# Performance work log

Measured on AMD Instinct MI355X. Metric: run time of the kernel, lower is better.

## Reference

```python
import jax, jax.numpy as jnp
import numpy as np

B = 8192; L = 50; D_EMB = 128
N_USER = 100000; N_MOVIE = 50000; N_DENSE = 8
D = 2 * D_EMB + D_EMB + N_DENSE  # 392 total_input_dim
E = 4; T = 2; H1 = 256; H2 = 128; ATT_H = 64; N_CROSS = 3


def setup_inputs() -> dict:
    key = jax.random.key(0)
    ks = jax.random.split(key, 28)
    rn = lambda k, shape, s=0.02: jax.random.normal(k, shape, jnp.float32) * s
    inp = {
        'userId': jax.random.randint(ks[0], (B,), 0, N_USER),
        'movieId': jax.random.randint(ks[1], (B,), 0, N_MOVIE),
        'seq_history': jax.random.randint(ks[2], (B, L), 0, N_MOVIE),
        'dense_feats': jax.random.normal(ks[3], (B, N_DENSE), jnp.float32),
        # embeddings (row 0 is padding_idx -> zeros)
        'emb_user': rn(ks[4], (N_USER + 1, D_EMB)).at[0].set(0.0),
        'emb_movie': rn(ks[5], (N_MOVIE + 1, D_EMB)).at[0].set(0.0),
        # DIN attention MLP: input [q,k,q-k,q*k] = 4*D_EMB
        'att_w1': rn(ks[6], (4 * D_EMB, ATT_H)), 'att_b1': jnp.zeros((ATT_H,), jnp.float32),
        'att_w2': rn(ks[7], (ATT_H, 1)), 'att_b2': jnp.zeros((1,), jnp.float32),
        # LayerNorms
        'in_gamma': jnp.ones((D,), jnp.float32), 'in_beta': jnp.zeros((D,), jnp.float32),
        'cr_gamma': jnp.ones((D,), jnp.float32), 'cr_beta': jnp.zeros((D,), jnp.float32),
        # CrossNetV2: x_{l+1} = x0 * (x_l W_l + b_l) + x_l
        'cross_W': rn(ks[8], (N_CROSS, D, D)), 'cross_b': jnp.zeros((N_CROSS, D), jnp.float32),
        # MMoE experts: Linear(D,H1)-ReLU-Linear(H1,H2), batched over E
        'exp_w1': rn(ks[9], (E, D, H1)), 'exp_b1': jnp.zeros((E, H1), jnp.float32),
        'exp_w2': rn(ks[10], (E, H1, H2)), 'exp_b2': jnp.zeros((E, H2), jnp.float32),
        # gates per task
        'gate_w': rn(ks[11], (T, D, E)), 'gate_b': jnp.zeros((T, E), jnp.float32),
        # task heads Linear(H2, 1)
        'head_w': rn(ks[12], (T, H2)), 'head_b': jnp.zeros((T,), jnp.float32),
    }
    return inp


def _layernorm(x, g, b, eps=1e-5):
    m = jnp.mean(x, axis=-1, keepdims=True)
    v = jnp.var(x, axis=-1, keepdims=True)
    return (x - m) * jax.lax.rsqrt(v + eps) * g + b


def _forward(userId, movieId, seq_history, dense_feats, emb_user, emb_movie,
             att_w1, att_b1, att_w2, att_b2, in_gamma, in_beta,
             cross_W, cross_b, cr_gamma, cr_beta,
             exp_w1, exp_b1, exp_w2, exp_b2, gate_w, gate_b, head_w, head_b):
    # sparse embedding gathers
    user_e = emb_user[userId]            # [B, D_EMB]
    movie_e = emb_movie[movieId]         # [B, D_EMB]  (target item)
    hist = emb_movie[seq_history]        # [B, L, D_EMB]
    mask = seq_history > 0               # [B, L]

    # DIN attention pooling
    q = jnp.broadcast_to(movie_e[:, None, :], hist.shape)            # [B, L, D_EMB]
    att_in = jnp.concatenate([q, hist, q - hist, q * hist], axis=-1)  # [B, L, 4*D_EMB]
    scores = (jax.nn.relu(att_in @ att_w1 + att_b1) @ att_w2 + att_b2)[..., 0]  # [B, L]
    scores = jnp.where(mask, scores, -1e9)
    probs = jax.nn.softmax(scores, axis=-1)                           # [B, L]
    interest = jnp.einsum('bl,bld->bd', probs, hist)                  # [B, D_EMB]

    x = jnp.concatenate([user_e, movie_e, interest, dense_feats], axis=-1)  # [B, D]
    x = _layernorm(x, in_gamma, in_beta)

    # CrossNetV2
    x0 = x
    for l in range(N_CROSS):
        x = x0 * (x @ cross_W[l] + cross_b[l]) + x
    x = _layernorm(x, cr_gamma, cr_beta)

    # MMoE: batched expert GEMMs + per-task soft gates
    h = jax.nn.relu(jnp.einsum('bd,edh->ebh', x, exp_w1) + exp_b1[:, None, :])  # [E,B,H1]
    eo = jnp.einsum('ebh,eho->ebo', h, exp_w2) + exp_b2[:, None, :]             # [E,B,H2]
    g = jax.nn.softmax(jnp.einsum('bd,tde->tbe', x, gate_w) + gate_b[:, None, :], axis=-1)  # [T,B,E]
    task_feat = jnp.einsum('tbe,ebo->tbo', g, eo)                                # [T,B,H2]

    logits = jnp.einsum('tbo,to->tb', task_feat, head_w) + head_b[:, None]       # [T,B]
    return logits


def reference(userId, movieId, seq_history, dense_feats, emb_user, emb_movie,
              att_w1, att_b1, att_w2, att_b2, in_gamma, in_beta,
              cross_W, cross_b, cr_gamma, cr_beta,
              exp_w1, exp_b1, exp_w2, exp_b2, gate_w, gate_b, head_w, head_b):
    return _forward(userId, movieId, seq_history, dense_feats, emb_user, emb_movie,
                    att_w1, att_b1, att_w2, att_b2, in_gamma, in_beta,
                    cross_W, cross_b, cr_gamma, cr_beta,
                    exp_w1, exp_b1, exp_w2, exp_b2, gate_w, gate_b, head_w, head_b)
```

## Files before the change

### kernel.cpp

```cpp
#include <hip/hip_runtime.h>
#include <hip/hip_bf16.h>

typedef short short8 __attribute__((ext_vector_type(8)));
typedef short short4v __attribute__((ext_vector_type(4)));
typedef float f32x4 __attribute__((ext_vector_type(4)));

constexpr int BB = 8192;
constexpr int LL = 50;
constexpr int DE = 128;
constexpr int DD = 392;
constexpr int HH1 = 256;
constexpr int HH2 = 128;

__device__ __forceinline__ short f2b(float x) {
    __hip_bfloat16 h = __float2bfloat16(x);
    return __builtin_bit_cast(short, h);
}
__device__ __forceinline__ float b2f(short v) {
    unsigned u = ((unsigned)(unsigned short)v) << 16;
    return __builtin_bit_cast(float, u);
}

__global__ __launch_bounds__(256) void prep_small(
    const float* __restrict__ w1,
    const float* __restrict__ w2, const float* __restrict__ b2,
    const float* __restrict__ head_w,
    short* __restrict__ WqpT, float* __restrict__ WkpFf,
    float* __restrict__ hw2, float* __restrict__ hc)
{
    __shared__ float hw[256];
    const int b = blockIdx.x, t = threadIdx.x;
    if (b < 32) {
        int o = b * 256 + t;
        int h = o >> 7, d = o & 127;
        WqpT[o] = f2b(w1[d * 64 + h] + w1[16384 + d * 64 + h]);
    } else if (b < 64) {
        int o = (b - 32) * 256 + t;
        int e = o & 7, lane = (o >> 3) & 63, nt = (o >> 9) & 3, kt = o >> 11;
        int k = (kt << 5) + ((lane >> 4) << 3) + e;
        int h = (nt << 4) + (lane & 15);
        int base = (o >> 3) << 4;
        WkpFf[base + e]     = w1[(128 + k) * 64 + h] - w1[(256 + k) * 64 + h];
        WkpFf[base + 8 + e] = w1[(384 + k) * 64 + h];
    } else {
        const int e = b - 64;
        hw[t] = head_w[t];
        __syncthreads();
        const float* row = &w2[((long)e * HH1 + t) * HH2];
        float s0 = 0.f, s1 = 0.f;
        #pragma unroll 8
        for (int o = 0; o < 128; o += 4) {
            float4 v = *reinterpret_cast<const float4*>(&row[o]);
            s0 += v.x * hw[o] + v.y * hw[o + 1] + v.z * hw[o + 2] + v.w * hw[o + 3];
            s1 += v.x * hw[128 + o] + v.y * hw[129 + o] + v.z * hw[130 + o] + v.w * hw[131 + o];
        }
        hw2[(((e << 8) + t) << 1) + 0] = s0;
        hw2[(((e << 8) + t) << 1) + 1] = s1;
        if (t < 2) {
            float s = 0.f;
            for (int o = 0; o < 128; ++o) s += b2[e * 128 + o] * hw[t * 128 + o];
            hc[e * 2 + t] = s;
        }
    }
}

constexpr int S0 = 3 * 392 * 392;
constexpr int S1 = 4 * 392 * 256;
constexpr int S2 = (50001 * 128) / 4;
constexpr int S3 = (BB * 128) / 4;

__global__ __launch_bounds__(256) void prep_trans(
    const float* __restrict__ cross_W, const float* __restrict__ exp_w1,
    const float* __restrict__ emb_movie, const int* __restrict__ movieId,
    short* __restrict__ WTc, short* __restrict__ WT1, short* __restrict__ embB,
    short* __restrict__ qb)
{
    int idx = blockIdx.x * 256 + threadIdx.x;
    if (idx < S0) {
        int z = idx / (392 * 392), rr = idx - z * 392 * 392;
        int c = rr / 392, r = rr - c * 392;
        WTc[idx] = f2b(cross_W[(long)z * 153664 + r * 392 + c]);
    } else if (idx < S0 + S1) {
        int j = idx - S0;
        int z = j / 100352, rr = j - z * 100352;
        int c = rr / 392, r = rr - c * 392;
        WT1[j] = f2b(exp_w1[(long)z * 100352 + r * 256 + c]);
    } else if (idx < S0 + S1 + S2) {
        long j = (long)(idx - S0 - S1) << 2;
        float4 v = *reinterpret_cast<const float4*>(&emb_movie[j]);
        short4v o;
        o[0] = f2b(v.x); o[1] = f2b(v.y); o[2] = f2b(v.z); o[3] = f2b(v.w);
        *reinterpret_cast<short4v*>(&embB[j]) = o;
    } else if (idx < S0 + S1 + S2 + S3) {
        int j = idx - S0 - S1 - S2;
        int bb = j >> 5, d0 = (j & 31) << 2;
        float4 v = *reinterpret_cast<const float4*>(
            &emb_movie[(long)movieId[bb] * DE + d0]);
        short4v o;
        o[0] = f2b(v.x); o[1] = f2b(v.y); o[2] = f2b(v.z); o[3] = f2b(v.w);
        *reinterpret_cast<short4v*>(&qb[bb * DE + d0]) = o;
    }
}

__global__ __launch_bounds__(256, 8) void attn_kernel(
    const int* __restrict__ userId, const int* __restrict__ movieId,
    const int* __restrict__ seq, const float* __restrict__ dense,
    const float* __restrict__ emb_user, const float* __restrict__ emb_movie,
    const short* __restrict__ embB,
    const float* __restrict__ qcAll, const float* __restrict__ WkpFf,
    const float* __restrict__ att_w2, const float* __restrict__ att_b2,
    const float* __restrict__ in_gamma, const float* __restrict__ in_beta,
    float* __restrict__ x0f, short* __restrict__ x0b)
{
    __shared__ short hist[64 * 128];
    __shared__ float qs[128];
    __shared__ int   seq_s[64];
    __shared__ float spS[4][64];
    __shared__ float probs[64];
    __shared__ float ibuf[4][128];
    __shared__ float stats[2];

    const int b = blockIdx.x;
    const int t = threadIdx.x;
    const int lane = t & 63;
    const int w = t >> 6;

    if (t < 128) qs[t] = emb_movie[(long)movieId[b] * DE + t];
    if (t < 64)  seq_s[t] = (t < LL) ? seq[b * LL + t] : 0;
    __syncthreads();

    #pragma unroll
    for (int i = 0; i < 4; ++i) {
        const int idx = t + (i << 8);
        const int l = idx >> 4, c = idx & 15;
        short8 hv = *reinterpret_cast<const short8*>(&embB[(long)seq_s[l] * DE + (c << 3)]);
        const int byte = (l << 8) + ((c << 4) ^ ((l & 7) << 4));
        *reinterpret_cast<short8*>(reinterpret_cast<char*>(hist) + byte) = hv;
    }

    const int col = (w << 4) + (lane & 15);
    float ue = (t < 128) ? emb_user[(long)userId[b] * DE + t] : 0.f;
    float dv = (t >= 128 && t < 136) ? dense[b * 8 + (t - 128)] : 0.f;
    const float qc  = qcAll[((long)b << 6) + col];
    const float w2v = att_w2[col];

    short8 bfrag[4];
    #pragma unroll
    for (int kt = 0; kt < 4; ++kt) {
        const float* wkp = &WkpFf[((((kt << 2) + w) << 6) | lane) << 4];
        const int kq = (kt << 5) + ((lane >> 4) << 3);
        #pragma unroll
        for (int j = 0; j < 8; ++j)
            bfrag[kt][j] = f2b(fmaf(qs[kq + j], wkp[8 + j], wkp[j]));
    }
    __syncthreads();

    #pragma unroll
    for (int mt = 0; mt < 4; ++mt) {
        f32x4 acc = {0.f, 0.f, 0.f, 0.f};
        const int row = (mt << 4) + (lane & 15);
        const int rbase = row << 8;
        const int swz = (row & 7) << 4;
        #pragma unroll
        for (int kt = 0; kt < 4; ++kt) {
            const int kbyte = (kt << 6) + ((lane >> 4) << 4);
            short8 a = *reinterpret_cast<const short8*>(
                reinterpret_cast<char*>(hist) + rbase + (kbyte ^ swz));
            acc = __builtin_amdgcn_mfma_f32_16x16x32_bf16(a, bfrag[kt], acc, 0, 0, 0);
        }
        #pragma unroll
        for (int r = 0; r < 4; ++r) {
            float v = fmaxf(acc[r] + qc, 0.f) * w2v;
            v += __shfl_xor(v, 1); v += __shfl_xor(v, 2);
            v += __shfl_xor(v, 4); v += __shfl_xor(v, 8);
            if ((lane & 15) == 0)
                spS[w][(mt << 4) + ((lane >> 4) << 2) + r] = v;
        }
    }
    __syncthreads();

    if (t < 64) {
        float sc = spS[0][t] + spS[1][t] + spS[2][t] + spS[3][t] + att_b2[0];
        float s = (t < LL) ? ((seq_s[t] > 0) ? sc : -1e9f) : -INFINITY;
        float m = s;
        #pragma unroll
        for (int off = 32; off > 0; off >>= 1) m = fmaxf(m, __shfl_xor(m, off));
        float e = (t < LL) ? __expf(s - m) : 0.f;
        float sum = e;
        #pragma unroll
        for (int off = 32; off > 0; off >>= 1) sum += __shfl_xor(sum, off);
        probs[t] = (t < LL) ? (e / sum) : 0.f;
    }
    __syncthreads();

    const int g  = t >> 5;
    const int d0 = (t & 31) << 2;
    float4 ps = make_float4(0.f, 0.f, 0.f, 0.f);
    #pragma unroll
    for (int i = 0; i < 8; ++i) {
        const int l = g + (i << 3);
        const int byte = (l << 8) + ((d0 << 1) ^ ((l & 7) << 4));
        short4v hv = *reinterpret_cast<const short4v*>(
            reinterpret_cast<const char*>(hist) + byte);
        const float p = probs[l];
        ps.x = fmaf(p, b2f(hv[0]), ps.x);
        ps.y = fmaf(p, b2f(hv[1]), ps.y);
        ps.z = fmaf(p, b2f(hv[2]), ps.z);
        ps.w = fmaf(p, b2f(hv[3]), ps.w);
    }
    ps.x += __shfl_xor(ps.x, 32); ps.y += __shfl_xor(ps.y, 32);
    ps.z += __shfl_xor(ps.z, 32); ps.w += __shfl_xor(ps.w, 32);
    if (lane < 32)
        *reinterpret_cast<float4*>(&ibuf[w][lane << 2]) = ps;
    __syncthreads();

    float v0 = (t < 128) ? ue : qs[t - 128];
    float v1 = 0.f;
    if (t < 128)       v1 = ibuf[0][t] + ibuf[1][t] + ibuf[2][t] + ibuf[3][t];
    else if (t < 136)  v1 = dv;

    float s2 = v0 + v1, q2 = v0 * v0 + v1 * v1;
    #pragma unroll
    for (int off = 32; off > 0; off >>= 1) {
        s2 += __shfl_xor(s2, off);
        q2 += __shfl_xor(q2, off);
    }
    if (lane == 0) { spS[0][w] = s2; spS[1][w] = q2; }
    __syncthreads();
    if (t == 0) {
        float S = spS[0][0] + spS[0][1] + spS[0][2] + spS[0][3];
        float Q = spS[1][0] + spS[1][1] + spS[1][2] + spS[1][3];
        float mean = S / (float)DD;
        float var = Q / (float)DD - mean * mean;
        stats[0] = mean;
        stats[1] = rsqrtf(var + 1e-5f);
    }
    __syncthreads();
    const float mean = stats[0], inv = stats[1];
    const long base = (long)b * DD;
    float o0 = (v0 - mean) * inv * in_gamma[t] + in_beta[t];
    x0f[base + t] = o0; x0b[base + t] = f2b(o0);
    if (t < 136) {
        float o1 = (v1 - mean) * inv * in_gamma[256 + t] + in_beta[256 + t];
        x0f[base + 256 + t] = o1; x0b[base + 256 + t] = f2b(o1);
    }
}

template<int MODE, int WF32, int WB16, int NXB, int NZB>
__global__ __launch_bounds__(256) void bgemm(
    const short* __restrict__ A, const short* __restrict__ WT,
    const float* __restrict__ bias,
    float* __restrict__ outF, short* __restrict__ outB,
    const float* __restrict__ x0, const float* __restrict__ xin,
    int M, int N, int K, long aZ, long wZ, long bZ, long oZ)
{
    __shared__ short As[2][64 * 64];
    __shared__ short Bs[2][64 * 64];

    int id = blockIdx.x;
    const int qq = (int)gridDim.x >> 3;
    id = (id & 7) * qq + (id >> 3);
    const int mb  = id / (NXB * NZB);
    const int rem = id - mb * (NXB * NZB);
    const int z   = rem / NXB;
    const int xb  = rem - z * NXB;

    A += (long)z * aZ; WT += (long)z * wZ; bias += (long)z * bZ;
    const long oz = (long)z * oZ;

    const int t = threadIdx.x, w = t >> 6, lane = t & 63;
    const int m0 = mb * 64, n0 = xb * 64;
    const int sm = t >> 3, sk8 = (t & 7) << 3;

    f32x4 acc[4];
    #pragma unroll
    for (int i = 0; i < 4; ++i) {
        #pragma unroll
        for (int r = 0; r < 4; ++r) acc[i][r] = 0.f;
    }

    const int nsteps = (K + 63) >> 6;
    short8 avA[2], bvA[2], avB[2], bvB[2];

    auto loadA = [&](int k0) {
        #pragma unroll
        for (int i = 0; i < 2; ++i) {
            const int r = sm + (i << 5);
            short8 zv = {0, 0, 0, 0, 0, 0, 0, 0};
            avA[i] = zv; bvA[i] = zv;
            if (k0 + sk8 < K) {
                avA[i] = *reinterpret_cast<const short8*>(&A[(long)(m0 + r) * K + k0 + sk8]);
                if (n0 + r < N)
                    bvA[i] = *reinterpret_cast<const short8*>(&WT[(long)(n0 + r) * K + k0 + sk8]);
            }
        }
    };
    auto loadB = [&](int k0) {
        #pragma unroll
        for (int i = 0; i < 2; ++i) {
            const int r = sm + (i << 5);
            short8 zv = {0, 0, 0, 0, 0, 0, 0, 0};
            avB[i] = zv; bvB[i] = zv;
            if (k0 + sk8 < K) {
                avB[i] = *reinterpret_cast<const short8*>(&A[(long)(m0 + r) * K + k0 + sk8]);
                if (n0 + r < N)
                    bvB[i] = *reinterpret_cast<const short8*>(&WT[(long)(n0 + r) * K + k0 + sk8]);
            }
        }
    };
    auto wrA = [&](int buf) {
        #pragma unroll
        for (int i = 0; i < 2; ++i) {
            const int r = sm + (i << 5);
            const int byte = (r << 7) + ((sk8 << 1) ^ ((r & 7) << 4));
            *reinterpret_cast<short8*>(reinterpret_cast<char*>(&As[buf][0]) + byte) = avA[i];
            *reinterpret_cast<short8*>(reinterpret_cast<char*>(&Bs[buf][0]) + byte) = bvA[i];
        }
    };
    auto wrB = [&](int buf) {
        #pragma unroll
        for (int i = 0; i < 2; ++i) {
            const int r = sm + (i << 5);
            const int byte = (r << 7) + ((sk8 << 1) ^ ((r & 7) << 4));
            *reinterpret_cast<short8*>(reinterpret_cast<char*>(&As[buf][0]) + byte) = avB[i];
            *reinterpret_cast<short8*>(reinterpret_cast<char*>(&Bs[buf][0]) + byte) = bvB[i];
        }
    };
    auto domfma = [&](int buf) {
        #pragma unroll
        for (int kt = 0; kt < 2; ++kt) {
            const int kbyte = (kt << 6) + ((lane >> 4) << 4);
            const int ar = (w << 4) + (lane & 15);
            short8 a = *reinterpret_cast<const short8*>(
                reinterpret_cast<char*>(&As[buf][0]) + (ar << 7) + (kbyte ^ ((ar & 7) << 4)));
            #pragma unroll
            for (int nt = 0; nt < 4; ++nt) {
                const int br = (nt << 4) + (lane & 15);
                short8 bb = *reinterpret_cast<const short8*>(
                    reinterpret_cast<char*>(&Bs[buf][0]) + (br << 7) + (kbyte ^ ((br & 7) << 4)));
                acc[nt] = __builtin_amdgcn_mfma_f32_16x16x32_bf16(a, bb, acc[nt], 0, 0, 0);
            }
        }
    };

    loadA(0);
    wrA(0);
    if (nsteps > 1) loadA(64);
    if (nsteps > 2) loadB(128);
    __syncthreads();

    int cur = 0, s = 0;
    while (s + 1 < nsteps) {
        domfma(cur);
        wrA(cur ^ 1);
        if (s + 3 < nsteps) loadA((s + 3) << 6);
        __syncthreads(); cur ^= 1; ++s;
        if (s + 1 < nsteps) {
            domfma(cur);
            wrB(cur ^ 1);
            if (s + 3 < nsteps) loadB((s + 3) << 6);
            __syncthreads(); cur ^= 1; ++s;
        }
    }
    domfma(cur);

    #pragma unroll
    for (int nt = 0; nt < 4; ++nt) {
        const int col = n0 + (nt << 4) + (lane & 15);
        if (col < N) {
            const float bv = bias[col];
            #pragma unroll
            for (int r = 0; r < 4; ++r) {
                const int row = m0 + (w << 4) + ((lane >> 4) << 2) + r;
                float v = acc[nt][r] + bv;
                if (MODE == 1) v = fmaxf(v, 0.f);
                const long o = (long)row * N + col;
                if (MODE == 2) v = x0[o] * v + xin[o];
                if (WF32) outF[oz + o] = v;
                if (WB16) outB[oz + o] = f2b(v);
            }
        }
    }
}

__global__ __launch_bounds__(256) void ln_kernel(
    const float* __restrict__ in,
    const float* __restrict__ gamma, const float* __restrict__ beta,
    float* __restrict__ outF, short* __restrict__ outB)
{
    __shared__ float red[2][4];
    __shared__ float stats[2];
    const int b = blockIdx.x, t = threadIdx.x, lane = t & 63, w = t >> 6;
    const long base = (long)b * DD;
    float v0 = in[base + t];
    float v1 = (t < 136) ? in[base + 256 + t] : 0.f;
    float s = v0 + v1, q2 = v0 * v0 + v1 * v1;
    #pragma unroll
    for (int off = 32; off > 0; off >>= 1) {
        s += __shfl_xor(s, off);
        q2 += __shfl_xor(q2, off);
    }
    if (lane == 0) { red[0][w] = s; red[1][w] = q2; }
    __syncthreads();
    if (t == 0) {
        float S = red[0][0] + red[0][1] + red[0][2] + red[0][3];
        float Q = red[1][0] + red[1][1] + red[1][2] + red[1][3];
        float mean = S / (float)DD;
        float var = Q / (float)DD - mean * mean;
        stats[0] = mean;
        stats[1] = rsqrtf(var + 1e-5f);
    }
    __syncthreads();
    const float mean = stats[0], inv = stats[1];
    float o0 = (v0 - mean) * inv * gamma[t] + beta[t];
    outF[base + t] = o0; outB[base + t] = f2b(o0);
    if (t < 136) {
        float o1 = (v1 - mean) * inv * gamma[256 + t] + beta[256 + t];
        outF[base + 256 + t] = o1; outB[base + 256 + t] = f2b(o1);
    }
}

__global__ __launch_bounds__(256) void final_kernel(
    const float* __restrict__ x, const short* __restrict__ h1,
    const float* __restrict__ hw2, const float* __restrict__ hc,
    const float* __restrict__ gate_w, const float* __restrict__ gate_b,
    const float* __restrict__ head_b, float* __restrict__ out)
{
    const int t = threadIdx.x, lane = t & 63, w = t >> 6;
    const int b = blockIdx.x * 4 + w;
    const float* xr = x + (long)b * DD;

    float xv[7];
    #pragma unroll
    for (int i = 0; i < 7; ++i) {
        int d = lane + (i << 6);
        xv[i] = (d < DD) ? xr[d] : 0.f;
    }

    float gl[8] = {0.f, 0.f, 0.f, 0.f, 0.f, 0.f, 0.f, 0.f};
    #pragma unroll
    for (int i = 0; i < 7; ++i) {
        int d = lane + (i << 6);
        if (d < DD) {
            float4 g0 = *reinterpret_cast<const float4*>(&gate_w[d << 2]);
            float4 g1 = *reinterpret_cast<const float4*>(&gate_w[1568 + (d << 2)]);
            gl[0] = fmaf(xv[i], g0.x, gl[0]); gl[1] = fmaf(xv[i], g0.y, gl[1]);
            gl[2] = fmaf(xv[i], g0.z, gl[2]); gl[3] = fmaf(xv[i], g0.w, gl[3]);
            gl[4] = fmaf(xv[i], g1.x, gl[4]); gl[5] = fmaf(xv[i], g1.y, gl[5]);
            gl[6] = fmaf(xv[i], g1.z, gl[6]); gl[7] = fmaf(xv[i], g1.w, gl[7]);
        }
    }

    float ed[8];
    #pragma unroll
    for (int e = 0; e < 4; ++e) {
        short4v hv = *reinterpret_cast<const short4v*>(
            &h1[((long)e * BB + b) * HH1 + (lane << 2)]);
        const float* hwp = &hw2[(((e << 8) + (lane << 2))) << 1];
        float4 w01 = *reinterpret_cast<const float4*>(hwp);
        float4 w23 = *reinterpret_cast<const float4*>(hwp + 4);
        float h0 = b2f(hv[0]), h1f = b2f(hv[1]), h2 = b2f(hv[2]), h3 = b2f(hv[3]);
        ed[e]     = fmaf(h0, w01.x, fmaf(h1f, w01.z, fmaf(h2, w23.x, h3 * w23.z)));
        ed[4 + e] = fmaf(h0, w01.y, fmaf(h1f, w01.w, fmaf(h2, w23.y, h3 * w23.w)));
    }

    #pragma unroll
    for (int v = 0; v < 8; ++v) {
        #pragma unroll
        for (int off = 32; off > 0; off >>= 1) {
            gl[v] += __shfl_xor(gl[v], off);
            ed[v] += __shfl_xor(ed[v], off);
        }
    }

    if (lane == 0) {
        float res[2];
        #pragma unroll
        for (int tt = 0; tt < 2; ++tt) {
            float lv[4], m = -1e30f;
            #pragma unroll
            for (int e = 0; e < 4; ++e) {
                lv[e] = gl[tt * 4 + e] + gate_b[tt * 4 + e];
                m = fmaxf(m, lv[e]);
            }
            float sum = 0.f, acc = 0.f;
            #pragma unroll
            for (int e = 0; e < 4; ++e) { lv[e] = __expf(lv[e] - m); sum += lv[e]; }
            #pragma unroll
            for (int e = 0; e < 4; ++e)
                acc = fmaf(lv[e], ed[tt * 4 + e] + hc[e * 2 + tt], acc);
            res[tt] = head_b[tt] + acc / sum;
        }
        out[b] = res[0];
        out[BB + b] = res[1];
    }
}

extern "C" void kernel_launch(void* const* d_in, const int* in_sizes, int n_in,
                              void* d_out, int out_size, void* d_ws, size_t ws_size,
                              hipStream_t stream) {
    const int*   userId    = (const int*)d_in[0];
    const int*   movieId   = (const int*)d_in[1];
    const int*   seq       = (const int*)d_in[2];
    const float* dense     = (const float*)d_in[3];
    const float* emb_user  = (const float*)d_in[4];
    const float* emb_movie = (const float*)d_in[5];
    const float* att_w1    = (const float*)d_in[6];
    const float* att_b1    = (const float*)d_in[7];
    const float* att_w2    = (const float*)d_in[8];
    const float* att_b2    = (const float*)d_in[9];
    const float* in_gamma  = (const float*)d_in[10];
    const float* in_beta   = (const float*)d_in[11];
    const float* cr_gamma  = (const float*)d_in[12];
    const float* cr_beta   = (const float*)d_in[13];
    const float* cross_W   = (const float*)d_in[14];
    const float* cross_b   = (const float*)d_in[15];
    const float* exp_w1    = (const float*)d_in[16];
    const float* exp_b1    = (const float*)d_in[17];
    const float* exp_w2    = (const float*)d_in[18];
    const float* exp_b2    = (const float*)d_in[19];
    const float* gate_w    = (const float*)d_in[20];
    const float* gate_b    = (const float*)d_in[21];
    const float* head_w    = (const float*)d_in[22];
    const float* head_b    = (const float*)d_in[23];
    float* outp = (float*)d_out;

    char* p = (char*)d_ws;
    auto alloc = [&](size_t bytes) -> char* {
        char* r = p; p += (bytes + 255) & ~(size_t)255; return r;
    };
    short* WqpT  = (short*)alloc(8192 * 2);
    float* WkpFf = (float*)alloc(16384 * 4);
    float* hw2 = (float*)alloc(2048 * 4);
    float* hc  = (float*)alloc(8 * 4);
    short* WTc = (short*)alloc((size_t)3 * 392 * 392 * 2);
    short* WT1 = (short*)alloc((size_t)4 * 256 * 392 * 2);
    short* embB = (short*)alloc((size_t)50001 * 128 * 2);
    short* qb   = (short*)alloc((size_t)BB * DE * 2);
    float* qcAll = (float*)alloc((size_t)BB * 64 * 4);
    float* x0f = (float*)alloc((size_t)BB * DD * 4);
    short* x0b = (short*)alloc((size_t)BB * DD * 2);
    float* xAf = (float*)alloc((size_t)BB * DD * 4);
    short* xAb = (short*)alloc((size_t)BB * DD * 2);
    float* xBf = (float*)alloc((size_t)BB * DD * 4);
    short* xBb = (short*)alloc((size_t)BB * DD * 2);
    short* h1b = (short*)alloc((size_t)4 * BB * HH1 * 2);

    prep_small<<<68, 256, 0, stream>>>(att_w1, exp_w2, exp_b2, head_w,
                                       WqpT, WkpFf, hw2, hc);
    prep_trans<<<(S0 + S1 + S2 + S3 + 255) / 256, 256, 0, stream>>>(
        cross_W, exp_w1, emb_movie, movieId, WTc, WT1, embB, qb);

    bgemm<0, 1, 0, 1, 1><<<128, 256, 0, stream>>>(
        qb, WqpT, att_b1, qcAll, nullptr, nullptr, nullptr,
        BB, 64, DE, 0, 0, 0, 0);

    attn_kernel<<<BB, 256, 0, stream>>>(userId, movieId, seq, dense,
                                        emb_user, emb_movie, embB,
                                        qcAll, WkpFf,
                                        att_w2, att_b2,
                                        in_gamma, in_beta, x0f, x0b);

    bgemm<2, 1, 1, 7, 1><<<896, 256, 0, stream>>>(x0b, WTc, cross_b, xAf, xAb,
                                                  x0f, x0f, BB, DD, DD, 0, 0, 0, 0);
    bgemm<2, 1, 1, 7, 1><<<896, 256, 0, stream>>>(xAb, WTc + 392 * 392, cross_b + 392,
                                                  xBf, xBb, x0f, xAf, BB, DD, DD, 0, 0, 0, 0);
    bgemm<2, 1, 0, 7, 1><<<896, 256, 0, stream>>>(xBb, WTc + 2 * 392 * 392, cross_b + 784,
                                                  xAf, nullptr, x0f, xBf, BB, DD, DD, 0, 0, 0, 0);

    ln_kernel<<<BB, 256, 0, stream>>>(xAf, cr_gamma, cr_beta, xBf, xBb);

    bgemm<1, 0, 1, 4, 4><<<2048, 256, 0, stream>>>(
        xBb, WT1, exp_b1, nullptr, h1b, nullptr, nullptr,
        BB, HH1, DD, 0, (long)HH1 * DD, HH1, (long)BB * HH1);

    final_kernel<<<BB / 4, 256, 0, stream>>>(xBf, h1b, hw2, hc,
                                             gate_w, gate_b, head_b, outp);

    (void)in_sizes; (void)n_in; (void)out_size; (void)ws_size;
}
```

Before: 177.2 us.

## Fuse last cross layer with LayerNorm and gate logits; trim attention and GEMM pipeline

Measured after the change: 182.3 us. 1.03x slower.

```diff
diff --git a/kernel.cpp b/kernel.cpp
--- a/kernel.cpp
+++ b/kernel.cpp
@@ -64,16 +64,17 @@
     }
 }
 
-constexpr int S0 = 3 * 392 * 392;
+constexpr int S0 = 2 * 392 * 392;
 constexpr int S1 = 4 * 392 * 256;
 constexpr int S2 = (50001 * 128) / 4;
 constexpr int S3 = (BB * 128) / 4;
+constexpr int S4 = 400 * 448;
 
 __global__ __launch_bounds__(256) void prep_trans(
     const float* __restrict__ cross_W, const float* __restrict__ exp_w1,
     const float* __restrict__ emb_movie, const int* __restrict__ movieId,
     short* __restrict__ WTc, short* __restrict__ WT1, short* __restrict__ embB,
-    short* __restrict__ qb)
+    short* __restrict__ qb, short* __restrict__ WT3)
 {
     int idx = blockIdx.x * 256 + threadIdx.x;
     if (idx < S0) {
@@ -99,6 +100,11 @@
         short4v o;
         o[0] = f2b(v.x); o[1] = f2b(v.y); o[2] = f2b(v.z); o[3] = f2b(v.w);
         *reinterpret_cast<short4v*>(&qb[bb * DE + d0]) = o;
+    } else if (idx < S0 + S1 + S2 + S3 + S4) {
+        int j = idx - S0 - S1 - S2 - S3;
+        int n = j / 448, k = j - n * 448;
+        WT3[j] = (n < 392 && k < 392)
+                 ? f2b(cross_W[2L * 153664 + (long)k * 392 + n]) : (short)0;
     }
 }
 
@@ -112,30 +118,36 @@
     const float* __restrict__ in_gamma, const float* __restrict__ in_beta,
     float* __restrict__ x0f, short* __restrict__ x0b)
 {
-    __shared__ short hist[64 * 128];
-    __shared__ float qs[128];
-    __shared__ int   seq_s[64];
-    __shared__ float spS[4][64];
-    __shared__ float probs[64];
-    __shared__ float ibuf[4][128];
-    __shared__ float stats[2];
+    __shared__ __align__(16) char lds[17408];
+    short* hist = reinterpret_cast<short*>(lds);
+    float* qs   = reinterpret_cast<float*>(lds + 13312);
+    float* spS  = reinterpret_cast<float*>(lds + 13824);
+    float* probs= reinterpret_cast<float*>(lds + 14848);
+    float* ibuf = reinterpret_cast<float*>(lds + 15104);
+    float* stats= reinterpret_cast<float*>(lds + 17152);
 
     const int b = blockIdx.x;
     const int t = threadIdx.x;
     const int lane = t & 63;
     const int w = t >> 6;
-
-    if (t < 128) qs[t] = emb_movie[(long)movieId[b] * DE + t];
-    if (t < 64)  seq_s[t] = (t < LL) ? seq[b * LL + t] : 0;
-    __syncthreads();
-
+    const int mid = movieId[b];
+
+    if (t < 32)
+        *reinterpret_cast<float4*>(&qs[t << 2]) =
+            *reinterpret_cast<const float4*>(&emb_movie[(long)mid * DE + (t << 2)]);
+
+    const int g0 = t >> 4, c = t & 15;
     #pragma unroll
     for (int i = 0; i < 4; ++i) {
-        const int idx = t + (i << 8);
-        const int l = idx >> 4, c = idx & 15;
-        short8 hv = *reinterpret_cast<const short8*>(&embB[(long)seq_s[l] * DE + (c << 3)]);
-        const int byte = (l << 8) + ((c << 4) ^ ((l & 7) << 4));
-        *reinterpret_cast<short8*>(reinterpret_cast<char*>(hist) + byte) = hv;
+        const int l = g0 + (i << 4);
+        if (l < 52) {
+            int sidx = (l < LL) ? (b * LL + l) : 0;
+            int sv = seq[sidx];
+            if (l >= LL) sv = 0;
+            short8 hv = *reinterpret_cast<const short8*>(&embB[(long)sv * DE + (c << 3)]);
+            const int byte = (l << 8) + ((c << 4) ^ ((l & 7) << 4));
+            *reinterpret_cast<short8*>(reinterpret_cast<char*>(hist) + byte) = hv;
+        }
     }
 
     const int col = (w << 4) + (lane & 15);
@@ -143,6 +155,10 @@
     float dv = (t >= 128 && t < 136) ? dense[b * 8 + (t - 128)] : 0.f;
     const float qc  = qcAll[((long)b << 6) + col];
     const float w2v = att_w2[col];
+    int mseq = 0;
+    if (t < LL) mseq = seq[b * LL + t];
+
+    __syncthreads();
 
     short8 bfrag[4];
     #pragma unroll
@@ -153,7 +169,6 @@
         for (int j = 0; j < 8; ++j)
             bfrag[kt][j] = f2b(fmaf(qs[kq + j], wkp[8 + j], wkp[j]));
     }
-    __syncthreads();
 
     #pragma unroll
     for (int mt = 0; mt < 4; ++mt) {
@@ -174,14 +189,14 @@
             v += __shfl_xor(v, 1); v += __shfl_xor(v, 2);
             v += __shfl_xor(v, 4); v += __shfl_xor(v, 8);
             if ((lane & 15) == 0)
-                spS[w][(mt << 4) + ((lane >> 4) << 2) + r] = v;
+                spS[(w << 6) + (mt << 4) + ((lane >> 4) << 2) + r] = v;
         }
     }
     __syncthreads();
 
     if (t < 64) {
-        float sc = spS[0][t] + spS[1][t] + spS[2][t] + spS[3][t] + att_b2[0];
-        float s = (t < LL) ? ((seq_s[t] > 0) ? sc : -1e9f) : -INFINITY;
+        float sc = spS[t] + spS[64 + t] + spS[128 + t] + spS[192 + t] + att_b2[0];
+        float s = (t < LL) ? ((mseq > 0) ? sc : -1e9f) : -INFINITY;
         float m = s;
         #pragma unroll
         for (int off = 32; off > 0; off >>= 1) m = fmaxf(m, __shfl_xor(m, off));
@@ -199,24 +214,26 @@
     #pragma unroll
     for (int i = 0; i < 8; ++i) {
         const int l = g + (i << 3);
-        const int byte = (l << 8) + ((d0 << 1) ^ ((l & 7) << 4));
-        short4v hv = *reinterpret_cast<const short4v*>(
-            reinterpret_cast<const char*>(hist) + byte);
-        const float p = probs[l];
-        ps.x = fmaf(p, b2f(hv[0]), ps.x);
-        ps.y = fmaf(p, b2f(hv[1]), ps.y);
-        ps.z = fmaf(p, b2f(hv[2]), ps.z);
-        ps.w = fmaf(p, b2f(hv[3]), ps.w);
+        if (l < LL) {
+            const int byte = (l << 8) + ((d0 << 1) ^ ((l & 7) << 4));
+            short4v hv = *reinterpret_cast<const short4v*>(
+                reinterpret_cast<const char*>(hist) + byte);
+            const float p = probs[l];
+            ps.x = fmaf(p, b2f(hv[0]), ps.x);
+            ps.y = fmaf(p, b2f(hv[1]), ps.y);
+            ps.z = fmaf(p, b2f(hv[2]), ps.z);
+            ps.w = fmaf(p, b2f(hv[3]), ps.w);
+        }
     }
     ps.x += __shfl_xor(ps.x, 32); ps.y += __shfl_xor(ps.y, 32);
     ps.z += __shfl_xor(ps.z, 32); ps.w += __shfl_xor(ps.w, 32);
     if (lane < 32)
-        *reinterpret_cast<float4*>(&ibuf[w][lane << 2]) = ps;
+        *reinterpret_cast<float4*>(&ibuf[(w << 7) + ((lane & 31) << 2)]) = ps;
     __syncthreads();
 
     float v0 = (t < 128) ? ue : qs[t - 128];
     float v1 = 0.f;
-    if (t < 128)       v1 = ibuf[0][t] + ibuf[1][t] + ibuf[2][t] + ibuf[3][t];
+    if (t < 128)       v1 = ibuf[t] + ibuf[128 + t] + ibuf[256 + t] + ibuf[384 + t];
     else if (t < 136)  v1 = dv;
 
     float s2 = v0 + v1, q2 = v0 * v0 + v1 * v1;
@@ -225,11 +242,11 @@
         s2 += __shfl_xor(s2, off);
         q2 += __shfl_xor(q2, off);
     }
-    if (lane == 0) { spS[0][w] = s2; spS[1][w] = q2; }
+    if (lane == 0) { spS[w] = s2; spS[64 + w] = q2; }
     __syncthreads();
     if (t == 0) {
-        float S = spS[0][0] + spS[0][1] + spS[0][2] + spS[0][3];
-        float Q = spS[1][0] + spS[1][1] + spS[1][2] + spS[1][3];
+        float S = spS[0] + spS[1] + spS[2] + spS[3];
+        float Q = spS[64] + spS[65] + spS[66] + spS[67];
         float mean = S / (float)DD;
         float var = Q / (float)DD - mean * mean;
         stats[0] = mean;
@@ -280,7 +297,7 @@
     }
 
     const int nsteps = (K + 63) >> 6;
-    short8 avA[2], bvA[2], avB[2], bvB[2];
+    short8 avA[2], bvA[2];
 
     auto loadA = [&](int k0) {
         #pragma unroll
@@ -295,19 +312,6 @@
             }
         }
     };
-    auto loadB = [&](int k0) {
-        #pragma unroll
-        for (int i = 0; i < 2; ++i) {
-            const int r = sm + (i << 5);
-            short8 zv = {0, 0, 0, 0, 0, 0, 0, 0};
-            avB[i] = zv; bvB[i] = zv;
-            if (k0 + sk8 < K) {
-                avB[i] = *reinterpret_cast<const short8*>(&A[(long)(m0 + r) * K + k0 + sk8]);
-                if (n0 + r < N)
-                    bvB[i] = *reinterpret_cast<const short8*>(&WT[(long)(n0 + r) * K + k0 + sk8]);
-            }
-        }
-    };
     auto wrA = [&](int buf) {
         #pragma unroll
         for (int i = 0; i < 2; ++i) {
@@ -315,15 +319,6 @@
             const int byte = (r << 7) + ((sk8 << 1) ^ ((r & 7) << 4));
             *reinterpret_cast<short8*>(reinterpret_cast<char*>(&As[buf][0]) + byte) = avA[i];
             *reinterpret_cast<short8*>(reinterpret_cast<char*>(&Bs[buf][0]) + byte) = bvA[i];
-        }
-    };
-    auto wrB = [&](int buf) {
-        #pragma unroll
-        for (int i = 0; i < 2; ++i) {
-            const int r = sm + (i << 5);
-            const int byte = (r << 7) + ((sk8 << 1) ^ ((r & 7) << 4));
-            *reinterpret_cast<short8*>(reinterpret_cast<char*>(&As[buf][0]) + byte) = avB[i];
-            *reinterpret_cast<short8*>(reinterpret_cast<char*>(&Bs[buf][0]) + byte) = bvB[i];
         }
     };
     auto domfma = [&](int buf) {
@@ -346,21 +341,15 @@
     loadA(0);
     wrA(0);
     if (nsteps > 1) loadA(64);
-    if (nsteps > 2) loadB(128);
-    __syncthreads();
-
-    int cur = 0, s = 0;
-    while (s + 1 < nsteps) {
+    __syncthreads();
+
+    int cur = 0;
+    for (int s = 0; s + 1 < nsteps; ++s) {
         domfma(cur);
         wrA(cur ^ 1);
-        if (s + 3 < nsteps) loadA((s + 3) << 6);
-        __syncthreads(); cur ^= 1; ++s;
-        if (s + 1 < nsteps) {
-            domfma(cur);
-            wrB(cur ^ 1);
-            if (s + 3 < nsteps) loadB((s + 3) << 6);
-            __syncthreads(); cur ^= 1; ++s;
-        }
+        if (s + 2 < nsteps) loadA((s + 2) << 6);
+        __syncthreads();
+        cur ^= 1;
     }
     domfma(cur);
 
@@ -383,73 +372,136 @@
     }
 }
 
-__global__ __launch_bounds__(256) void ln_kernel(
-    const float* __restrict__ in,
+__global__ __launch_bounds__(256, 2) void cross3_ln(
+    const short* __restrict__ Ab,
+    const short* __restrict__ WT3,
+    const float* __restrict__ bias,
+    const float* __restrict__ x0f, const float* __restrict__ xinf,
     const float* __restrict__ gamma, const float* __restrict__ beta,
-    float* __restrict__ outF, short* __restrict__ outB)
+    const float* __restrict__ gate_w,
+    short* __restrict__ outB,
+    float* __restrict__ glog)
 {
-    __shared__ float red[2][4];
-    __shared__ float stats[2];
-    const int b = blockIdx.x, t = threadIdx.x, lane = t & 63, w = t >> 6;
-    const long base = (long)b * DD;
-    float v0 = in[base + t];
-    float v1 = (t < 136) ? in[base + 256 + t] : 0.f;
-    float s = v0 + v1, q2 = v0 * v0 + v1 * v1;
-    #pragma unroll
-    for (int off = 32; off > 0; off >>= 1) {
-        s += __shfl_xor(s, off);
-        q2 += __shfl_xor(q2, off);
-    }
-    if (lane == 0) { red[0][w] = s; red[1][w] = q2; }
-    __syncthreads();
-    if (t == 0) {
-        float S = red[0][0] + red[0][1] + red[0][2] + red[0][3];
-        float Q = red[1][0] + red[1][1] + red[1][2] + red[1][3];
-        float mean = S / (float)DD;
-        float var = Q / (float)DD - mean * mean;
-        stats[0] = mean;
-        stats[1] = rsqrtf(var + 1e-5f);
-    }
-    __syncthreads();
-    const float mean = stats[0], inv = stats[1];
-    float o0 = (v0 - mean) * inv * gamma[t] + beta[t];
-    outF[base + t] = o0; outB[base + t] = f2b(o0);
-    if (t < 136) {
-        float o1 = (v1 - mean) * inv * gamma[256 + t] + beta[256 + t];
-        outF[base + 256 + t] = o1; outB[base + 256 + t] = f2b(o1);
+    __shared__ float rowbuf[16][400];
+
+    int id = blockIdx.x;
+    id = (id & 7) * 64 + (id >> 3);
+    const int r0 = id << 4;
+
+    const int t = threadIdx.x, w = t >> 6, lane = t & 63;
+    const int arow = r0 + (lane & 15);
+    const int koff = (lane >> 4) << 3;
+
+    f32x4 acc[7];
+    #pragma unroll
+    for (int j = 0; j < 7; ++j) {
+        #pragma unroll
+        for (int r = 0; r < 4; ++r) acc[j][r] = 0.f;
+    }
+
+    for (int k0 = 0; k0 < 384; k0 += 64) {
+        short8 a0 = *reinterpret_cast<const short8*>(&Ab[(long)arow * DD + k0 + koff]);
+        short8 a1 = *reinterpret_cast<const short8*>(&Ab[(long)arow * DD + k0 + 32 + koff]);
+        #pragma unroll
+        for (int j = 0; j < 7; ++j) {
+            const int nt = w + (j << 2);
+            if (nt < 25) {
+                const int brow = (nt << 4) + (lane & 15);
+                short8 b0 = *reinterpret_cast<const short8*>(&WT3[(long)brow * 448 + k0 + koff]);
+                short8 b1 = *reinterpret_cast<const short8*>(&WT3[(long)brow * 448 + k0 + 32 + koff]);
+                acc[j] = __builtin_amdgcn_mfma_f32_16x16x32_bf16(a0, b0, acc[j], 0, 0, 0);
+                acc[j] = __builtin_amdgcn_mfma_f32_16x16x32_bf16(a1, b1, acc[j], 0, 0, 0);
+            }
+        }
+    }
+    {
+        short8 a0 = {0, 0, 0, 0, 0, 0, 0, 0};
+        if (koff == 0)
+            a0 = *reinterpret_cast<const short8*>(&Ab[(long)arow * DD + 384]);
+        #pragma unroll
+        for (int j = 0; j < 7; ++j) {
+            const int nt = w + (j << 2);
+            if (nt < 25) {
+                const int brow = (nt << 4) + (lane & 15);
+                short8 b0 = *reinterpret_cast<const short8*>(&WT3[(long)brow * 448 + 384 + koff]);
+                acc[j] = __builtin_amdgcn_mfma_f32_16x16x32_bf16(a0, b0, acc[j], 0, 0, 0);
+            }
+        }
+    }
+
+    #pragma unroll
+    for (int j = 0; j < 7; ++j) {
+        const int nt = w + (j << 2);
+        if (nt < 25) {
+            const int col = (nt << 4) + (lane & 15);
+            if (col < DD) {
+                const float bv = bias[col];
+                #pragma unroll
+                for (int r = 0; r < 4; ++r) {
+                    const int lr = ((lane >> 4) << 2) + r;
+                    const long o = (long)(r0 + lr) * DD + col;
+                    rowbuf[lr][col] = x0f[o] * (acc[j][r] + bv) + xinf[o];
+                }
+            }
+        }
+    }
+    __syncthreads();
+
+    #pragma unroll
+    for (int rr = 0; rr < 4; ++rr) {
+        const int lr = (w << 2) + rr;
+        const int gr = r0 + lr;
+        float vals[7];
+        float s = 0.f, q = 0.f;
+        #pragma unroll
+        for (int jj = 0; jj < 7; ++jj) {
+            const int cc = lane + (jj << 6);
+            float v = (cc < DD) ? rowbuf[lr][cc] : 0.f;
+            vals[jj] = v;
+            s += v; q += v * v;
+        }
+        #pragma unroll
+        for (int off = 32; off > 0; off >>= 1) {
+            s += __shfl_xor(s, off);
+            q += __shfl_xor(q, off);
+        }
+        const float mean = s / (float)DD;
+        const float inv = rsqrtf(q / (float)DD - mean * mean + 1e-5f);
+        float gp[8] = {0.f, 0.f, 0.f, 0.f, 0.f, 0.f, 0.f, 0.f};
+        #pragma unroll
+        for (int jj = 0; jj < 7; ++jj) {
+            const int cc = lane + (jj << 6);
+            if (cc < DD) {
+                float xn = (vals[jj] - mean) * inv * gamma[cc] + beta[cc];
+                outB[(long)gr * DD + cc] = f2b(xn);
+                float4 g0 = *reinterpret_cast<const float4*>(&gate_w[cc << 2]);
+                float4 g1 = *reinterpret_cast<const float4*>(&gate_w[1568 + (cc << 2)]);
+                gp[0] = fmaf(xn, g0.x, gp[0]); gp[1] = fmaf(xn, g0.y, gp[1]);
+                gp[2] = fmaf(xn, g0.z, gp[2]); gp[3] = fmaf(xn, g0.w, gp[3]);
+                gp[4] = fmaf(xn, g1.x, gp[4]); gp[5] = fmaf(xn, g1.y, gp[5]);
+                gp[6] = fmaf(xn, g1.z, gp[6]); gp[7] = fmaf(xn, g1.w, gp[7]);
+            }
+        }
+        #pragma unroll
+        for (int v = 0; v < 8; ++v) {
+            #pragma unroll
+            for (int off = 32; off > 0; off >>= 1) gp[v] += __shfl_xor(gp[v], off);
+        }
+        if (lane == 0) {
+            #pragma unroll
+            for (int v = 0; v < 8; ++v) glog[((long)gr << 3) + v] = gp[v];
+        }
     }
 }
 
 __global__ __launch_bounds__(256) void final_kernel(
-    const float* __restrict__ x, const short* __restrict__ h1,
+    const float* __restrict__ glog, const short* __restrict__ h1,
     const float* __restrict__ hw2, const float* __restrict__ hc,
-    const float* __restrict__ gate_w, const float* __restrict__ gate_b,
-    const float* __restrict__ head_b, float* __restrict__ out)
+    const float* __restrict__ gate_b, const float* __restrict__ head_b,
+    float* __restrict__ out)
 {
     const int t = threadIdx.x, lane = t & 63, w = t >> 6;
     const int b = blockIdx.x * 4 + w;
-    const float* xr = x + (long)b * DD;
-
-    float xv[7];
-    #pragma unroll
-    for (int i = 0; i < 7; ++i) {
-        int d = lane + (i << 6);
-        xv[i] = (d < DD) ? xr[d] : 0.f;
-    }
-
-    float gl[8] = {0.f, 0.f, 0.f, 0.f, 0.f, 0.f, 0.f, 0.f};
-    #pragma unroll
-    for (int i = 0; i < 7; ++i) {
-        int d = lane + (i << 6);
-        if (d < DD) {
-            float4 g0 = *reinterpret_cast<const float4*>(&gate_w[d << 2]);
-            float4 g1 = *reinterpret_cast<const float4*>(&gate_w[1568 + (d << 2)]);
-            gl[0] = fmaf(xv[i], g0.x, gl[0]); gl[1] = fmaf(xv[i], g0.y, gl[1]);
-            gl[2] = fmaf(xv[i], g0.z, gl[2]); gl[3] = fmaf(xv[i], g0.w, gl[3]);
-            gl[4] = fmaf(xv[i], g1.x, gl[4]); gl[5] = fmaf(xv[i], g1.y, gl[5]);
-            gl[6] = fmaf(xv[i], g1.z, gl[6]); gl[7] = fmaf(xv[i], g1.w, gl[7]);
-        }
-    }
 
     float ed[8];
     #pragma unroll
@@ -463,17 +515,16 @@
         ed[e]     = fmaf(h0, w01.x, fmaf(h1f, w01.z, fmaf(h2, w23.x, h3 * w23.z)));
         ed[4 + e] = fmaf(h0, w01.y, fmaf(h1f, w01.w, fmaf(h2, w23.y, h3 * w23.w)));
     }
-
     #pragma unroll
     for (int v = 0; v < 8; ++v) {
         #pragma unroll
-        for (int off = 32; off > 0; off >>= 1) {
-            gl[v] += __shfl_xor(gl[v], off);
-            ed[v] += __shfl_xor(ed[v], off);
-        }
+        for (int off = 32; off > 0; off >>= 1) ed[v] += __shfl_xor(ed[v], off);
     }
 
     if (lane == 0) {
+        float4 gA = *reinterpret_cast<const float4*>(&glog[(long)b << 3]);
+        float4 gB = *reinterpret_cast<const float4*>(&glog[((long)b << 3) + 4]);
+        float gl[8] = {gA.x, gA.y, gA.z, gA.w, gB.x, gB.y, gB.z, gB.w};
         float res[2];
         #pragma unroll
         for (int tt = 0; tt < 2; ++tt) {
@@ -533,8 +584,9 @@
     float* WkpFf = (float*)alloc(16384 * 4);
     float* hw2 = (float*)alloc(2048 * 4);
     float* hc  = (float*)alloc(8 * 4);
-    short* WTc = (short*)alloc((size_t)3 * 392 * 392 * 2);
+    short* WTc = (short*)alloc((size_t)2 * 392 * 392 * 2);
     short* WT1 = (short*)alloc((size_t)4 * 256 * 392 * 2);
+    short* WT3 = (short*)alloc((size_t)400 * 448 * 2);
     short* embB = (short*)alloc((size_t)50001 * 128 * 2);
     short* qb   = (short*)alloc((size_t)BB * DE * 2);
     float* qcAll = (float*)alloc((size_t)BB * 64 * 4);
@@ -544,12 +596,14 @@
     short* xAb = (short*)alloc((size_t)BB * DD * 2);
     float* xBf = (float*)alloc((size_t)BB * DD * 4);
     short* xBb = (short*)alloc((size_t)BB * DD * 2);
+    short* xCb = (short*)alloc((size_t)BB * DD * 2);
+    float* glog = (float*)alloc((size_t)BB * 8 * 4);
     short* h1b = (short*)alloc((size_t)4 * BB * HH1 * 2);
 
     prep_small<<<68, 256, 0, stream>>>(att_w1, exp_w2, exp_b2, head_w,
                                        WqpT, WkpFf, hw2, hc);
-    prep_trans<<<(S0 + S1 + S2 + S3 + 255) / 256, 256, 0, stream>>>(
-        cross_W, exp_w1, emb_movie, movieId, WTc, WT1, embB, qb);
+    prep_trans<<<(S0 + S1 + S2 + S3 + S4 + 255) / 256, 256, 0, stream>>>(
+        cross_W, exp_w1, emb_movie, movieId, WTc, WT1, embB, qb, WT3);
 
     bgemm<0, 1, 0, 1, 1><<<128, 256, 0, stream>>>(
         qb, WqpT, att_b1, qcAll, nullptr, nullptr, nullptr,
@@ -557,25 +611,23 @@
 
     attn_kernel<<<BB, 256, 0, stream>>>(userId, movieId, seq, dense,
                                         emb_user, emb_movie, embB,
-                                        qcAll, WkpFf,
-                                        att_w2, att_b2,
+                                        qcAll, WkpFf, att_w2, att_b2,
                                         in_gamma, in_beta, x0f, x0b);
 
     bgemm<2, 1, 1, 7, 1><<<896, 256, 0, stream>>>(x0b, WTc, cross_b, xAf, xAb,
                                                   x0f, x0f, BB, DD, DD, 0, 0, 0, 0);
     bgemm<2, 1, 1, 7, 1><<<896, 256, 0, stream>>>(xAb, WTc + 392 * 392, cross_b + 392,
                                                   xBf, xBb, x0f, xAf, BB, DD, DD, 0, 0, 0, 0);
-    bgemm<2, 1, 0, 7, 1><<<896, 256, 0, stream>>>(xBb, WTc + 2 * 392 * 392, cross_b + 784,
-                                                  xAf, nullptr, x0f, xBf, BB, DD, DD, 0, 0, 0, 0);
-
-    ln_kernel<<<BB, 256, 0, stream>>>(xAf, cr_gamma, cr_beta, xBf, xBb);
+
+    cross3_ln<<<512, 256, 0, stream>>>(xBb, WT3, cross_b + 784, x0f, xBf,
+                                       cr_gamma, cr_beta, gate_w, xCb, glog);
 
     bgemm<1, 0, 1, 4, 4><<<2048, 256, 0, stream>>>(
-        xBb, WT1, exp_b1, nullptr, h1b, nullptr, nullptr,
+        xCb, WT1, exp_b1, nullptr, h1b, nullptr, nullptr,
         BB, HH1, DD, 0, (long)HH1 * DD, HH1, (long)BB * HH1);
 
-    final_kernel<<<BB / 4, 256, 0, stream>>>(xBf, h1b, hw2, hc,
-                                             gate_w, gate_b, head_b, outp);
+    final_kernel<<<BB / 4, 256, 0, stream>>>(glog, h1b, hw2, hc,
+                                             gate_b, head_b, outp);
 
     (void)in_sizes; (void)n_in; (void)out_size; (void)ws_size;
 }
```
